# Kernel tuning notes

Measured on AMD Instinct MI355X. Metric: run time of the kernel, lower is better.

## Reference

```python
import jax, jax.numpy as jnp
import numpy as np

B, L, D, H, K_DELAYS = 8, 2048, 512, 8, 8
DH = D // H


def setup_inputs() -> dict:
    key = jax.random.key(0)
    ks = jax.random.split(key, 6)
    def lin_w(k):
        return 0.02 * jax.random.normal(k, (D, D), jnp.float32)
    return {
        "x_q":  jax.random.normal(ks[0], (B, L, D), jnp.float32),
        "x_kv": jax.random.normal(ks[1], (B, L, D), jnp.float32),
        "Wq": lin_w(ks[2]), "bq": jnp.zeros((D,), jnp.float32),
        "Wk": lin_w(ks[3]), "bk": jnp.zeros((D,), jnp.float32),
        "Wv": lin_w(ks[4]), "bv": jnp.zeros((D,), jnp.float32),
        "Wo": lin_w(ks[5]), "bo": jnp.zeros((D,), jnp.float32),
    }


def reference(x_q, x_kv, Wq, bq, Wk, bk, Wv, bv, Wo, bo):
    Bx, Lx, Dx = x_q.shape

    def proj(x, W, b):  # torch Linear: x @ W.T + b, then split heads -> [B,H,L,dh]
        return (x @ W.T + b).reshape(Bx, Lx, H, DH).transpose(0, 2, 1, 3)

    q = proj(x_q, Wq, bq)
    k = proj(x_kv, Wk, bk)
    v = proj(x_kv, Wv, bv)

    # FFT-based autocorrelation over the time axis (axis=2)
    qz = q - q.mean(axis=2, keepdims=True)
    kz = k - k.mean(axis=2, keepdims=True)
    Qf = jnp.fft.rfft(qz, axis=2)
    Kf = jnp.fft.rfft(kz, axis=2)
    corr = jnp.fft.irfft(Qf * jnp.conj(Kf), n=Lx, axis=2).mean(axis=-1)  # [B,H,L]
    # torch expands corr to [B,H,Lq,Lk] then means over Lq -> identical to corr
    score = corr

    K = min(K_DELAYS, Lx)
    vals, idx = jax.lax.top_k(score, K)                    # [B,H,K]
    w = vals / (vals.sum(axis=-1, keepdims=True) + 1e-12)
    w = jax.lax.stop_gradient(w)                           # .detach() in torch

    # circular shift by -delay == gather at (t + delay) mod L
    t = jnp.arange(Lx)
    pos = (t[None, None, None, :] + idx[..., None]) % Lx   # [B,H,K,L]
    v_sh = jnp.take_along_axis(v[:, :, None, :, :], pos[..., None], axis=3)  # [B,H,K,L,dh]
    out = jnp.einsum('bhk,bhkld->bhld', w, v_sh)           # weighted sum over delays

    out = out.transpose(0, 2, 1, 3).reshape(Bx, Lx, Dx)
    return out @ Wo.T + bo
```

## Files before the change

### kernel.cpp

```cpp
#include <hip/hip_runtime.h>
#include <math.h>

#define BB 8
#define LL 2048
#define DD 512
#define HH 8
#define DHH 64
#define KD 8
#define MM (BB*LL)

typedef _Float16 f16x2 __attribute__((ext_vector_type(2)));
typedef _Float16 f16x4 __attribute__((ext_vector_type(4)));
typedef _Float16 f16x8 __attribute__((ext_vector_type(8)));
typedef float    f32x4 __attribute__((ext_vector_type(4)));

__device__ inline void cvt8(const float* __restrict__ s, _Float16* hp, _Float16* lp) {
    const float4 a = *(const float4*)s;
    const float4 b = *(const float4*)(s + 4);
    const float v[8] = {a.x, a.y, a.z, a.w, b.x, b.y, b.z, b.w};
    f16x8 hi, lo;
#pragma unroll
    for (int j = 0; j < 8; j++) {
        const _Float16 h = (_Float16)v[j];
        hi[j] = h;
        lo[j] = (_Float16)((v[j] - (float)h) * 512.0f);
    }
    *(f16x8*)hp = hi;
    if (lp) *(f16x8*)lp = lo;
}

__global__ __launch_bounds__(256) void prep_w(const float* __restrict__ Wq, const float* __restrict__ Wk,
                                              const float* __restrict__ Wv, const float* __restrict__ Wo,
                                              _Float16* __restrict__ Wq_h, _Float16* __restrict__ Wq_l,
                                              _Float16* __restrict__ Wk_h, _Float16* __restrict__ Wk_l,
                                              _Float16* __restrict__ Wv_h, _Float16* __restrict__ Wo_h) {
    const int g = blockIdx.x * 256 + threadIdx.x;
    const int which = g >> 15;
    const size_t idx = (size_t)(g & 32767) * 8;
    if (which == 0)      cvt8(Wq + idx, Wq_h + idx, Wq_l + idx);
    else if (which == 1) cvt8(Wk + idx, Wk_h + idx, Wk_l + idx);
    else if (which == 2) cvt8(Wv + idx, Wv_h + idx, nullptr);
    else                 cvt8(Wo + idx, Wo_h + idx, nullptr);
}

__device__ __forceinline__ void stage16(const _Float16* g, const _Float16* l) {
    __builtin_amdgcn_global_load_lds(
        (const __attribute__((address_space(1))) void*)g,
        (__attribute__((address_space(3))) void*)l,
        16, 0, 0);
}

template<int NPROD, int MODE, int AF32, int BK>
__device__ __forceinline__ void gemm_body(const float* __restrict__ A32,
                                          const _Float16* __restrict__ Ag,
                                          const _Float16* __restrict__ Al_g,
                                          const _Float16* __restrict__ Bg,
                                          const _Float16* __restrict__ Bl_g,
                                          const float* __restrict__ bias,
                                          void* __restrict__ Cv,
                                          _Float16* lds, int l0) {
    constexpr int CPR  = BK / 8;
    constexpr int NST  = BK / 16;
    constexpr int SH   = (BK == 32) ? 2 : 3;
    constexpr int PLN  = 128 * BK;

#define SWZR(R) ((BK == 32) ? (((R) >> 1) & 3) : ((R) & 7))
#define ASWZ(R, g) ((size_t)(R) * BK + (size_t)((((g) ^ SWZR(R))) * 8))

    _Float16* Ah = lds;
    _Float16* Bh = lds + PLN;
    _Float16* Al = (NPROD == 3) ? lds + 2 * PLN : lds;
    _Float16* Bl = (NPROD == 3) ? lds + 3 * PLN : lds;

    const int t  = threadIdx.x;
    const int m0 = (((l0 >> 5) << 3) | (l0 & 7)) * 128;
    const int n0 = ((l0 >> 3) & 3) * 128;

    const int wv   = t >> 6;
    const int lane = t & 63;
    const int wm   = (wv >> 1) * 64;
    const int wn   = (wv & 1) * 64;
    const int lm   = lane & 15;
    const int quad = lane >> 4;

    int srow[NST], schk[NST], sgrp[NST];
#pragma unroll
    for (int i = 0; i < NST; i++) {
        const int s = (i * 4 + wv) * 64 + lane;
        srow[i] = s >> SH;
        schk[i] = (s & (CPR - 1)) ^ SWZR(srow[i]);
        sgrp[i] = (i * 4 + wv) * 512;
    }

    f32x4 acc0[4][4] = {};
    f32x4 acc1[4][4] = {};

    float4 vaA[NST], vaB[NST];
    if (AF32) {
#pragma unroll
        for (int i = 0; i < NST; i++) {
            const float* src = A32 + (size_t)(m0 + srow[i]) * 512 + schk[i] * 8;
            vaA[i] = *(const float4*)src;
            vaB[i] = *(const float4*)(src + 4);
        }
    }

    for (int k0 = 0; k0 < 512; k0 += BK) {
        __syncthreads();
#pragma unroll
        for (int i = 0; i < NST; i++) {
            const size_t offB = (size_t)(n0 + srow[i]) * 512 + k0 + schk[i] * 8;
            stage16(Bg + offB, Bh + sgrp[i]);
            if (NPROD == 3) stage16(Bl_g + offB, Bl + sgrp[i]);
            if (AF32) {
                const float va[8] = {vaA[i].x, vaA[i].y, vaA[i].z, vaA[i].w,
                                     vaB[i].x, vaB[i].y, vaB[i].z, vaB[i].w};
                f16x8 hi, lo;
#pragma unroll
                for (int j = 0; j < 8; j++) {
                    const _Float16 h = (_Float16)va[j];
                    hi[j] = h;
                    if (NPROD == 3) lo[j] = (_Float16)((va[j] - (float)h) * 512.0f);
                }
                *(f16x8*)&Ah[sgrp[i] + lane * 8] = hi;
                if (NPROD == 3) *(f16x8*)&Al[sgrp[i] + lane * 8] = lo;
            } else {
                const size_t offA = (size_t)(m0 + srow[i]) * 512 + k0 + schk[i] * 8;
                stage16(Ag + offA, Ah + sgrp[i]);
                if (NPROD == 3) stage16(Al_g + offA, Al + sgrp[i]);
            }
        }
        __syncthreads();

        if (AF32 && k0 + BK < 512) {
#pragma unroll
            for (int i = 0; i < NST; i++) {
                const float* src = A32 + (size_t)(m0 + srow[i]) * 512 + (k0 + BK) + schk[i] * 8;
                vaA[i] = *(const float4*)src;
                vaB[i] = *(const float4*)(src + 4);
            }
        }

#pragma unroll
        for (int ks = 0; ks < BK / 32; ks++) {
            const int gq = ks * 4 + quad;
            f16x8 afh[4], bf[4];
#pragma unroll
            for (int mt = 0; mt < 4; mt++)
                afh[mt] = *(f16x8*)&Ah[ASWZ(wm + mt * 16 + lm, gq)];
#pragma unroll
            for (int nt = 0; nt < 4; nt++)
                bf[nt] = *(f16x8*)&Bh[ASWZ(wn + nt * 16 + lm, gq)];

#pragma unroll
            for (int mt = 0; mt < 4; mt++)
#pragma unroll
                for (int nt = 0; nt < 4; nt++)
                    acc0[mt][nt] = __builtin_amdgcn_mfma_f32_16x16x32_f16(afh[mt], bf[nt], acc0[mt][nt], 0, 0, 0);

            if (NPROD == 3) {
                f16x8 afl[4];
#pragma unroll
                for (int mt = 0; mt < 4; mt++)
                    afl[mt] = *(f16x8*)&Al[ASWZ(wm + mt * 16 + lm, gq)];
#pragma unroll
                for (int mt = 0; mt < 4; mt++)
#pragma unroll
                    for (int nt = 0; nt < 4; nt++)
                        acc1[mt][nt] = __builtin_amdgcn_mfma_f32_16x16x32_f16(afl[mt], bf[nt], acc1[mt][nt], 0, 0, 0);
#pragma unroll
                for (int nt = 0; nt < 4; nt++)
                    bf[nt] = *(f16x8*)&Bl[ASWZ(wn + nt * 16 + lm, gq)];
#pragma unroll
                for (int mt = 0; mt < 4; mt++)
#pragma unroll
                    for (int nt = 0; nt < 4; nt++)
                        acc1[mt][nt] = __builtin_amdgcn_mfma_f32_16x16x32_f16(afh[mt], bf[nt], acc1[mt][nt], 0, 0, 0);
            }
        }
    }
#undef ASWZ
#undef SWZR

#pragma unroll
    for (int mt = 0; mt < 4; mt++) {
#pragma unroll
        for (int nt = 0; nt < 4; nt++) {
            const int n = n0 + wn + nt * 16 + lm;
            const float bv = bias[n];
            float val[4];
#pragma unroll
            for (int r = 0; r < 4; r++) {
                val[r] = acc0[mt][nt][r] + bv;
                if (NPROD == 3) val[r] += acc1[mt][nt][r] * (1.0f / 512.0f);
            }
            const int mbase = m0 + wm + mt * 16 + quad * 4;
            const int b_idx = mbase >> 11;
            const int lbase = mbase & 2047;
            if (MODE == 0) {
                float* C = (float*)Cv;
#pragma unroll
                for (int r = 0; r < 4; r++) C[(size_t)(mbase + r) * 512 + n] = val[r];
            } else if (MODE == 1) {
                float* C = (float*)Cv;
                float4 pv = make_float4(val[0], val[1], val[2], val[3]);
                *(float4*)&C[((size_t)(b_idx * 512 + n)) * 2048 + lbase] = pv;
            } else {
                _Float16* C = (_Float16*)Cv;
#pragma unroll
                for (int r = 0; r < 4; r++)
                    C[(size_t)b_idx * 1048576 + (size_t)(n >> 6) * 131072
                      + (size_t)(lbase + r) * 64 + (n & 63)] = (_Float16)val[r];
            }
        }
    }
}

__global__ __launch_bounds__(256, 2) void gemm_qk(const float* __restrict__ A0f,
                                                  const _Float16* __restrict__ B0h, const _Float16* __restrict__ B0l,
                                                  const float* __restrict__ bias0, float* __restrict__ C0,
                                                  const float* __restrict__ A1f,
                                                  const _Float16* __restrict__ B1h, const _Float16* __restrict__ B1l,
                                                  const float* __restrict__ bias1, float* __restrict__ C1) {
    __shared__ __align__(16) _Float16 lds[32768];
    const int prob = blockIdx.x >> 9;
    const int l0   = blockIdx.x & 511;
    if (prob == 0)
        gemm_body<3, 1, 1, 64>(A0f, nullptr, nullptr, B0h, B0l, bias0, C0, lds, l0);
    else
        gemm_body<3, 1, 1, 64>(A1f, nullptr, nullptr, B1h, B1l, bias1, C1, lds, l0);
}

__global__ __launch_bounds__(256, 3) void gemm_o(const _Float16* __restrict__ Ah_g,
                                                 const _Float16* __restrict__ Bh_g,
                                                 const float* __restrict__ bias,
                                                 float* __restrict__ C) {
    __shared__ __align__(16) _Float16 lds[16384];
    gemm_body<1, 0, 0, 64>(nullptr, Ah_g, Ah_g, Bh_g, Bh_g, bias, C, lds, blockIdx.x);
}

#define PAD3(i) ((i) + ((i) >> 3))

__device__ inline float2 cmul2(float2 a, float2 w) {
    return make_float2(a.x * w.x - a.y * w.y, a.x * w.y + a.y * w.x);
}
__device__ inline float2 cadd2(float2 a, float2 b) { return make_float2(a.x + b.x, a.y + b.y); }
__device__ inline float2 csub2(float2 a, float2 b) { return make_float2(a.x - b.x, a.y - b.y); }

__global__ __launch_bounds__(256) void fft_fwd(const float* __restrict__ qT,
                                               const float* __restrict__ kT,
                                               float* __restrict__ specP) {
    const int blk  = blockIdx.x;
    const int bh   = blk >> 4;
    const int part = blk & 15;
    const int t    = threadIdx.x;
    __shared__ float2 Zs[2304];
    __shared__ float2 Wt[1024];

#pragma unroll
    for (int s = 0; s < 4; s++) {
        const int j = t + s * 256;
        float sv, cv;
        __sincosf(2.0f * (float)M_PI * (float)j / 2048.0f, &sv, &cv);
        Wt[j] = make_float2(cv, -sv);
    }

    float2 pacc[8];
#pragma unroll
    for (int s = 0; s < 8; s++) pacc[s] = make_float2(0.0f, 0.0f);

    const int low5 = t & 31, hi3 = t >> 5;
    const int low2 = t & 3,  hi6 = t >> 2;

    float2 zn[8];
    {
        const int seq0 = bh * 64 + part * 4;
        const float* qp = qT + (size_t)seq0 * 2048;
        const float* kp = kT + (size_t)seq0 * 2048;
#pragma unroll
        for (int s = 0; s < 8; s++) zn[s] = make_float2(qp[t + 256 * s], kp[t + 256 * s]);
    }

    for (int j4 = 0; j4 < 4; j4++) {
        float2 z[8];
#pragma unroll
        for (int s = 0; s < 8; s++) z[s] = zn[s];
        if (j4 + 1 < 4) {
            const int seq = bh * 64 + part * 4 + j4 + 1;
            const float* qp = qT + (size_t)seq * 2048;
            const float* kp = kT + (size_t)seq * 2048;
#pragma unroll
            for (int s = 0; s < 8; s++) zn[s] = make_float2(qp[t + 256 * s], kp[t + 256 * s]);
        }
        __syncthreads();

#pragma unroll
        for (int sp = 0; sp < 4; sp++) {
            float2 u = z[sp], v = z[sp + 4];
            z[sp]     = cadd2(u, v);
            z[sp + 4] = cmul2(csub2(u, v), Wt[t + 256 * sp]);
        }
#pragma unroll
        for (int base = 0; base < 8; base += 4)
#pragma unroll
            for (int q2 = 0; q2 < 2; q2++) {
                float2 u = z[base + q2], v = z[base + q2 + 2];
                z[base + q2]     = cadd2(u, v);
                z[base + q2 + 2] = cmul2(csub2(u, v), Wt[2 * (t + 256 * q2)]);
            }
        {
            const float2 w = Wt[4 * t];
#pragma unroll
            for (int e = 0; e < 8; e += 2) {
                float2 u = z[e], v = z[e + 1];
                z[e]     = cadd2(u, v);
                z[e + 1] = cmul2(csub2(u, v), w);
            }
        }

#pragma unroll
        for (int s = 0; s < 8; s++) Zs[PAD3(t + 256 * s)] = z[s];
        __syncthreads();
#pragma unroll
        for (int s = 0; s < 8; s++) z[s] = Zs[PAD3(low5 + 32 * s + 256 * hi3)];

#pragma unroll
        for (int sp = 0; sp < 4; sp++) {
            float2 u = z[sp], v = z[sp + 4];
            z[sp]     = cadd2(u, v);
            z[sp + 4] = cmul2(csub2(u, v), Wt[8 * (low5 + 32 * sp)]);
        }
#pragma unroll
        for (int base = 0; base < 8; base += 4)
#pragma unroll
            for (int q2 = 0; q2 < 2; q2++) {
                float2 u = z[base + q2], v = z[base + q2 + 2];
                z[base + q2]     = cadd2(u, v);
                z[base + q2 + 2] = cmul2(csub2(u, v), Wt[16 * (low5 + 32 * q2)]);
            }
        {
            const float2 w = Wt[32 * low5];
#pragma unroll
            for (int e = 0; e < 8; e += 2) {
                float2 u = z[e], v = z[e + 1];
                z[e]     = cadd2(u, v);
                z[e + 1] = cmul2(csub2(u, v), w);
            }
        }

#pragma unroll
        for (int s = 0; s < 8; s++) Zs[PAD3(low5 + 32 * s + 256 * hi3)] = z[s];
        __syncthreads();
#pragma unroll
        for (int s = 0; s < 8; s++) z[s] = Zs[PAD3(low2 + 4 * s + 32 * hi6)];

#pragma unroll
        for (int sp = 0; sp < 4; sp++) {
            float2 u = z[sp], v = z[sp + 4];
            z[sp]     = cadd2(u, v);
            z[sp + 4] = cmul2(csub2(u, v), Wt[64 * (low2 + 4 * sp)]);
        }
#pragma unroll
        for (int base = 0; base < 8; base += 4)
#pragma unroll
            for (int q2 = 0; q2 < 2; q2++) {
                float2 u = z[base + q2], v = z[base + q2 + 2];
                z[base + q2]     = cadd2(u, v);
                z[base + q2 + 2] = cmul2(csub2(u, v), Wt[128 * (low2 + 4 * q2)]);
            }
        {
            const float2 w = Wt[256 * low2];
#pragma unroll
            for (int e = 0; e < 8; e += 2) {
                float2 u = z[e], v = z[e + 1];
                z[e]     = cadd2(u, v);
                z[e + 1] = cmul2(csub2(u, v), w);
            }
        }

#pragma unroll
        for (int s = 0; s < 8; s++) Zs[PAD3(low2 + 4 * s + 32 * hi6)] = z[s];
        __syncthreads();
#pragma unroll
        for (int s = 0; s < 8; s++) z[s] = Zs[PAD3(8 * t + s)];

#pragma unroll
        for (int base = 0; base < 8; base += 4) {
            {
                float2 u = z[base], v = z[base + 2];
                z[base]     = cadd2(u, v);
                z[base + 2] = csub2(u, v);
            }
            {
                float2 u = z[base + 1], v = z[base + 3];
                float2 d = csub2(u, v);
                z[base + 1] = cadd2(u, v);
                z[base + 3] = make_float2(d.y, -d.x);
            }
        }
#pragma unroll
        for (int e = 0; e < 8; e += 2) {
            float2 u = z[e], v = z[e + 1];
            z[e]     = cadd2(u, v);
            z[e + 1] = csub2(u, v);
        }

#pragma unroll
        for (int s = 0; s < 8; s++) Zs[PAD3(8 * t + s)] = z[s];
        __syncthreads();

#pragma unroll
        for (int s = 0; s < 8; s++) {
            const int p  = t + 256 * s;
            const int f  = (int)(__brev((unsigned)p) >> 21);
            const int fm = (2048 - f) & 2047;
            const int p2 = (int)(__brev((unsigned)fm) >> 21);
            const float2 zf = Zs[PAD3(p)];
            const float2 zm = Zs[PAD3(p2)];
            const float qr = 0.5f * (zf.x + zm.x);
            const float qi = 0.5f * (zf.y - zm.y);
            const float kr = 0.5f * (zf.y + zm.y);
            const float ki = 0.5f * (zm.x - zf.x);
            if (f != 0) {
                pacc[s].x += qr * kr + qi * ki;
                pacc[s].y += qi * kr - qr * ki;
            }
        }
    }

    float2* outp = (float2*)specP + (size_t)blk * 2048;
#pragma unroll
    for (int s = 0; s < 8; s++) outp[t + 256 * s] = pacc[s];
}

__device__ inline void build_twiddle(float2* Wt, int tid, float sign) {
#pragma unroll
    for (int s = 0; s < 4; s++) {
        const int j = tid + s * 256;
        const float a = 2.0f * (float)M_PI * (float)j / 2048.0f;
        float sv, cv;
        __sincosf(a, &sv, &cv);
        Wt[j] = make_float2(cv, sign * sv);
    }
}

__device__ inline void fft2048_stages(float2* Z, const float2* Wt, int tid) {
    for (int st = 0; st < 11; st++) {
        const int half = 1 << st;
        const int shift = 10 - st;
#pragma unroll
        for (int r = 0; r < 4; r++) {
            const int m   = tid + r * 256;
            const int grp = m >> st;
            const int pos = m & (half - 1);
            const int i0  = (grp << (st + 1)) + pos;
            const int i1  = i0 + half;
            const float2 w = Wt[pos << shift];
            const float2 a = Z[i0];
            const float2 b = Z[i1];
            const float tr = b.x * w.x - b.y * w.y;
            const float ti = b.x * w.y + b.y * w.x;
            Z[i0] = make_float2(a.x + tr, a.y + ti);
            Z[i1] = make_float2(a.x - tr, a.y - ti);
        }
        __syncthreads();
    }
}

__global__ __launch_bounds__(256, 3) void gemm_v_fftinv(const float* __restrict__ xkv,
                                                        const _Float16* __restrict__ Bh_g,
                                                        const float* __restrict__ bias,
                                                        _Float16* __restrict__ C,
                                                        const float* __restrict__ specP,
                                                        int* __restrict__ delays,
                                                        float* __restrict__ weights) {
    __shared__ __align__(16) char smem[24608];
    const int bid = blockIdx.x;
    const int tid = threadIdx.x;

    if (bid >= 64) {
        gemm_body<1, 2, 1, 32>(xkv, nullptr, nullptr, Bh_g, Bh_g, bias, C, (_Float16*)smem, bid - 64);
        return;
    }

    const int bh = bid;
    float2* Z  = (float2*)smem;
    float2* Wt = (float2*)(smem + 16384);
    float*  wvs = (float*)(smem + 24576);
    int*    wis = (int*)(smem + 24592);

    build_twiddle(Wt, tid, +1.0f);

    const float2* sp = (const float2*)specP + (size_t)bh * 16 * 2048;
#pragma unroll
    for (int s = 0; s < 8; s++) {
        const int p = tid + s * 256;
        float2 acc = make_float2(0.0f, 0.0f);
#pragma unroll
        for (int part = 0; part < 16; part++) {
            const float2 v = sp[part * 2048 + p];
            acc.x += v.x; acc.y += v.y;
        }
        Z[p] = acc;
    }
    __syncthreads();
    fft2048_stages(Z, Wt, tid);

    const float scale = 1.0f / (2048.0f * 64.0f);
    float cv[8];
#pragma unroll
    for (int s = 0; s < 8; s++) cv[s] = Z[tid + s * 256].x * scale;

    float bkv[KD];
    int   bki[KD];
#pragma unroll
    for (int k = 0; k < KD; k++) {
        float lv = -1e30f;
        int   li = 1 << 30;
#pragma unroll
        for (int s = 0; s < 8; s++) {
            const int idx = tid + s * 256;
            if (cv[s] > lv || (cv[s] == lv && idx < li)) { lv = cv[s]; li = idx; }
        }
#pragma unroll
        for (int off = 1; off < 64; off <<= 1) {
            const float v2 = __shfl_xor(lv, off);
            const int   i2 = __shfl_xor(li, off);
            if (v2 > lv || (v2 == lv && i2 < li)) { lv = v2; li = i2; }
        }
        if ((tid & 63) == 0) { wvs[tid >> 6] = lv; wis[tid >> 6] = li; }
        __syncthreads();
        float bv = wvs[0];
        int   bi = wis[0];
#pragma unroll
        for (int j = 1; j < 4; j++) {
            const float v2 = wvs[j];
            const int   i2 = wis[j];
            if (v2 > bv || (v2 == bv && i2 < bi)) { bv = v2; bi = i2; }
        }
        bkv[k] = bv;
        bki[k] = bi;
        if ((bi & 255) == tid) {
            const int slot = bi >> 8;
#pragma unroll
            for (int s = 0; s < 8; s++)
                if (s == slot) cv[s] = -1e30f;
        }
        __syncthreads();
    }

    if (tid == 0) {
        float sum = 0.0f;
#pragma unroll
        for (int k = 0; k < KD; k++) sum += bkv[k];
        const float inv = 1.0f / (sum + 1e-12f);
#pragma unroll
        for (int k = 0; k < KD; k++) {
            weights[bh * KD + k] = bkv[k] * inv;
            delays[bh * KD + k]  = bki[k];
        }
    }
}

__global__ __launch_bounds__(256) void gather_ws(const _Float16* __restrict__ v,
                                                 const int* __restrict__ delays,
                                                 const float* __restrict__ weights,
                                                 _Float16* __restrict__ outb) {
    const int gp = blockIdx.x * 256 + threadIdx.x;
    const int c8 = gp & 63;
    const int m  = gp >> 6;
    const int l  = m & 2047;
    const int b  = m >> 11;
    const int ch = c8 * 8;
    const int h  = ch >> 6;
    const int dh = ch & 63;
    const int bh = b * 8 + h;

    const _Float16* vb = v + (size_t)bh * 131072;
    float a[8] = {};
#pragma unroll
    for (int k = 0; k < KD; k++) {
        const int   d = delays[bh * KD + k];
        const float w = weights[bh * KD + k];
        const int   p = (l + d) & 2047;
        const f16x8 pv = *(const f16x8*)&vb[p * 64 + dh];
#pragma unroll
        for (int j = 0; j < 8; j++) a[j] = fmaf(w, (float)pv[j], a[j]);
    }
    f16x8 ov;
#pragma unroll
    for (int j = 0; j < 8; j++) ov[j] = (_Float16)a[j];
    *(f16x8*)&outb[(size_t)m * 512 + ch] = ov;
}

extern "C" void kernel_launch(void* const* d_in, const int* in_sizes, int n_in,
                              void* d_out, int out_size, void* d_ws, size_t ws_size,
                              hipStream_t stream) {
    const float* x_q  = (const float*)d_in[0];
    const float* x_kv = (const float*)d_in[1];
    const float* Wq   = (const float*)d_in[2];
    const float* bq   = (const float*)d_in[3];
    const float* Wk   = (const float*)d_in[4];
    const float* bk   = (const float*)d_in[5];
    const float* Wv   = (const float*)d_in[6];
    const float* bv   = (const float*)d_in[7];
    const float* Wo   = (const float*)d_in[8];
    const float* bo   = (const float*)d_in[9];
    float* out = (float*)d_out;

    char* ws = (char*)d_ws;
    float*    kf32  = (float*)   (ws + 0);
    _Float16* vh    = (_Float16*)(ws + 33554432);
    float*    specP = (float*)   (ws + 50331648);
    _Float16* gbuf  = (_Float16*)(ws + 67108864);
    _Float16* Wq_h  = (_Float16*)(ws + 83886080);
    _Float16* Wq_l  = (_Float16*)(ws + 84410368);
    _Float16* Wk_h  = (_Float16*)(ws + 84934656);
    _Float16* Wk_l  = (_Float16*)(ws + 85458944);
    _Float16* Wv_h  = (_Float16*)(ws + 85983232);
    _Float16* Wo_h  = (_Float16*)(ws + 86507520);
    int*      dely  = (int*)     (ws + 87031808);
    float*    wgt   = (float*)   (ws + 87033856);
    float*    qf32  = (float*)d_out;

    dim3 blk(256);

    prep_w<<<dim3(512), blk, 0, stream>>>(Wq, Wk, Wv, Wo,
                                          Wq_h, Wq_l, Wk_h, Wk_l, Wv_h, Wo_h);

    gemm_qk<<<dim3(1024), blk, 0, stream>>>(x_q,  Wq_h, Wq_l, bq, qf32,
                                            x_kv, Wk_h, Wk_l, bk, kf32);

    fft_fwd<<<dim3(1024), blk, 0, stream>>>(qf32, kf32, specP);

    gemm_v_fftinv<<<dim3(576), blk, 0, stream>>>(x_kv, Wv_h, bv, vh, specP, dely, wgt);

    gather_ws<<<dim3(4096), blk, 0, stream>>>(vh, dely, wgt, gbuf);

    gemm_o<<<dim3(512), blk, 0, stream>>>(gbuf, Wo_h, bo, out);
}
```

Baseline: 255.0 us.

## Fuse weight conversion into QK projection GEMM and drop prep kernel

The separate prep_w kernel is removed. The Q/K projection GEMM now reads fp32 weights directly and splits them into hi/lo fp16 in registers before writing to LDS, the same way it already handles the activations. Wv/Wo conversion runs in 256 extra blocks appended to the gemm_qk grid. This saves one kernel launch and the round trip of the converted Q/K weights through memory, but every GEMM block now redoes the weight conversion and issues twice as many fp32 B loads.

```diff
diff --git a/kernel.cpp b/kernel.cpp
--- a/kernel.cpp
+++ b/kernel.cpp
@@ -29,20 +29,6 @@
     if (lp) *(f16x8*)lp = lo;
 }
 
-__global__ __launch_bounds__(256) void prep_w(const float* __restrict__ Wq, const float* __restrict__ Wk,
-                                              const float* __restrict__ Wv, const float* __restrict__ Wo,
-                                              _Float16* __restrict__ Wq_h, _Float16* __restrict__ Wq_l,
-                                              _Float16* __restrict__ Wk_h, _Float16* __restrict__ Wk_l,
-                                              _Float16* __restrict__ Wv_h, _Float16* __restrict__ Wo_h) {
-    const int g = blockIdx.x * 256 + threadIdx.x;
-    const int which = g >> 15;
-    const size_t idx = (size_t)(g & 32767) * 8;
-    if (which == 0)      cvt8(Wq + idx, Wq_h + idx, Wq_l + idx);
-    else if (which == 1) cvt8(Wk + idx, Wk_h + idx, Wk_l + idx);
-    else if (which == 2) cvt8(Wv + idx, Wv_h + idx, nullptr);
-    else                 cvt8(Wo + idx, Wo_h + idx, nullptr);
-}
-
 __device__ __forceinline__ void stage16(const _Float16* g, const _Float16* l) {
     __builtin_amdgcn_global_load_lds(
         (const __attribute__((address_space(1))) void*)g,
@@ -50,10 +36,11 @@
         16, 0, 0);
 }
 
-template<int NPROD, int MODE, int AF32, int BK>
+template<int NPROD, int MODE, int AF32, int BF32, int BK>
 __device__ __forceinline__ void gemm_body(const float* __restrict__ A32,
                                           const _Float16* __restrict__ Ag,
                                           const _Float16* __restrict__ Al_g,
+                                          const float* __restrict__ B32,
                                           const _Float16* __restrict__ Bg,
                                           const _Float16* __restrict__ Bl_g,
                                           const float* __restrict__ bias,
@@ -95,7 +82,7 @@
     f32x4 acc0[4][4] = {};
     f32x4 acc1[4][4] = {};
 
-    float4 vaA[NST], vaB[NST];
+    float4 vaA[NST], vaB[NST], vbA[NST], vbB[NST];
     if (AF32) {
 #pragma unroll
         for (int i = 0; i < NST; i++) {
@@ -104,14 +91,36 @@
             vaB[i] = *(const float4*)(src + 4);
         }
     }
+    if (BF32) {
+#pragma unroll
+        for (int i = 0; i < NST; i++) {
+            const float* src = B32 + (size_t)(n0 + srow[i]) * 512 + schk[i] * 8;
+            vbA[i] = *(const float4*)src;
+            vbB[i] = *(const float4*)(src + 4);
+        }
+    }
 
     for (int k0 = 0; k0 < 512; k0 += BK) {
         __syncthreads();
 #pragma unroll
         for (int i = 0; i < NST; i++) {
-            const size_t offB = (size_t)(n0 + srow[i]) * 512 + k0 + schk[i] * 8;
-            stage16(Bg + offB, Bh + sgrp[i]);
-            if (NPROD == 3) stage16(Bl_g + offB, Bl + sgrp[i]);
+            if (BF32) {
+                const float vb[8] = {vbA[i].x, vbA[i].y, vbA[i].z, vbA[i].w,
+                                     vbB[i].x, vbB[i].y, vbB[i].z, vbB[i].w};
+                f16x8 hi, lo;
+#pragma unroll
+                for (int j = 0; j < 8; j++) {
+                    const _Float16 h = (_Float16)vb[j];
+                    hi[j] = h;
+                    if (NPROD == 3) lo[j] = (_Float16)((vb[j] - (float)h) * 512.0f);
+                }
+                *(f16x8*)&Bh[sgrp[i] + lane * 8] = hi;
+                if (NPROD == 3) *(f16x8*)&Bl[sgrp[i] + lane * 8] = lo;
+            } else {
+                const size_t offB = (size_t)(n0 + srow[i]) * 512 + k0 + schk[i] * 8;
+                stage16(Bg + offB, Bh + sgrp[i]);
+                if (NPROD == 3) stage16(Bl_g + offB, Bl + sgrp[i]);
+            }
             if (AF32) {
                 const float va[8] = {vaA[i].x, vaA[i].y, vaA[i].z, vaA[i].w,
                                      vaB[i].x, vaB[i].y, vaB[i].z, vaB[i].w};
@@ -132,12 +141,22 @@
         }
         __syncthreads();
 
-        if (AF32 && k0 + BK < 512) {
-#pragma unroll
-            for (int i = 0; i < NST; i++) {
-                const float* src = A32 + (size_t)(m0 + srow[i]) * 512 + (k0 + BK) + schk[i] * 8;
-                vaA[i] = *(const float4*)src;
-                vaB[i] = *(const float4*)(src + 4);
+        if (k0 + BK < 512) {
+            if (AF32) {
+#pragma unroll
+                for (int i = 0; i < NST; i++) {
+                    const float* src = A32 + (size_t)(m0 + srow[i]) * 512 + (k0 + BK) + schk[i] * 8;
+                    vaA[i] = *(const float4*)src;
+                    vaB[i] = *(const float4*)(src + 4);
+                }
+            }
+            if (BF32) {
+#pragma unroll
+                for (int i = 0; i < NST; i++) {
+                    const float* src = B32 + (size_t)(n0 + srow[i]) * 512 + (k0 + BK) + schk[i] * 8;
+                    vbA[i] = *(const float4*)src;
+                    vbB[i] = *(const float4*)(src + 4);
+                }
             }
         }
 
@@ -217,18 +236,29 @@
 }
 
 __global__ __launch_bounds__(256, 2) void gemm_qk(const float* __restrict__ A0f,
-                                                  const _Float16* __restrict__ B0h, const _Float16* __restrict__ B0l,
+                                                  const float* __restrict__ W0f,
                                                   const float* __restrict__ bias0, float* __restrict__ C0,
                                                   const float* __restrict__ A1f,
-                                                  const _Float16* __restrict__ B1h, const _Float16* __restrict__ B1l,
-                                                  const float* __restrict__ bias1, float* __restrict__ C1) {
+                                                  const float* __restrict__ W1f,
+                                                  const float* __restrict__ bias1, float* __restrict__ C1,
+                                                  const float* __restrict__ Wv, const float* __restrict__ Wo,
+                                                  _Float16* __restrict__ Wv_h, _Float16* __restrict__ Wo_h) {
     __shared__ __align__(16) _Float16 lds[32768];
-    const int prob = blockIdx.x >> 9;
-    const int l0   = blockIdx.x & 511;
+    const int bid = blockIdx.x;
+    if (bid >= 1024) {
+        const int g = (bid - 1024) * 256 + threadIdx.x;
+        const int which = g >> 15;
+        const size_t idx = (size_t)(g & 32767) * 8;
+        if (which == 0) cvt8(Wv + idx, Wv_h + idx, nullptr);
+        else            cvt8(Wo + idx, Wo_h + idx, nullptr);
+        return;
+    }
+    const int prob = bid >> 9;
+    const int l0   = bid & 511;
     if (prob == 0)
-        gemm_body<3, 1, 1, 64>(A0f, nullptr, nullptr, B0h, B0l, bias0, C0, lds, l0);
+        gemm_body<3, 1, 1, 1, 64>(A0f, nullptr, nullptr, W0f, nullptr, nullptr, bias0, C0, lds, l0);
     else
-        gemm_body<3, 1, 1, 64>(A1f, nullptr, nullptr, B1h, B1l, bias1, C1, lds, l0);
+        gemm_body<3, 1, 1, 1, 64>(A1f, nullptr, nullptr, W1f, nullptr, nullptr, bias1, C1, lds, l0);
 }
 
 __global__ __launch_bounds__(256, 3) void gemm_o(const _Float16* __restrict__ Ah_g,
@@ -236,7 +266,7 @@
                                                  const float* __restrict__ bias,
                                                  float* __restrict__ C) {
     __shared__ __align__(16) _Float16 lds[16384];
-    gemm_body<1, 0, 0, 64>(nullptr, Ah_g, Ah_g, Bh_g, Bh_g, bias, C, lds, blockIdx.x);
+    gemm_body<1, 0, 0, 0, 64>(nullptr, Ah_g, Ah_g, nullptr, Bh_g, Bh_g, bias, C, lds, blockIdx.x);
 }
 
 #define PAD3(i) ((i) + ((i) >> 3))
@@ -479,7 +509,8 @@
     const int tid = threadIdx.x;
 
     if (bid >= 64) {
-        gemm_body<1, 2, 1, 32>(xkv, nullptr, nullptr, Bh_g, Bh_g, bias, C, (_Float16*)smem, bid - 64);
+        gemm_body<1, 2, 1, 0, 32>(xkv, nullptr, nullptr, nullptr, Bh_g, Bh_g, bias, C,
+                                  (_Float16*)smem, bid - 64);
         return;
     }
 
@@ -613,23 +644,17 @@
     _Float16* vh    = (_Float16*)(ws + 33554432);
     float*    specP = (float*)   (ws + 50331648);
     _Float16* gbuf  = (_Float16*)(ws + 67108864);
-    _Float16* Wq_h  = (_Float16*)(ws + 83886080);
-    _Float16* Wq_l  = (_Float16*)(ws + 84410368);
-    _Float16* Wk_h  = (_Float16*)(ws + 84934656);
-    _Float16* Wk_l  = (_Float16*)(ws + 85458944);
-    _Float16* Wv_h  = (_Float16*)(ws + 85983232);
-    _Float16* Wo_h  = (_Float16*)(ws + 86507520);
-    int*      dely  = (int*)     (ws + 87031808);
-    float*    wgt   = (float*)   (ws + 87033856);
+    _Float16* Wv_h  = (_Float16*)(ws + 83886080);
+    _Float16* Wo_h  = (_Float16*)(ws + 84410368);
+    int*      dely  = (int*)     (ws + 84934656);
+    float*    wgt   = (float*)   (ws + 84936704);
     float*    qf32  = (float*)d_out;
 
     dim3 blk(256);
 
-    prep_w<<<dim3(512), blk, 0, stream>>>(Wq, Wk, Wv, Wo,
-                                          Wq_h, Wq_l, Wk_h, Wk_l, Wv_h, Wo_h);
-
-    gemm_qk<<<dim3(1024), blk, 0, stream>>>(x_q,  Wq_h, Wq_l, bq, qf32,
-                                            x_kv, Wk_h, Wk_l, bk, kf32);
+    gemm_qk<<<dim3(1280), blk, 0, stream>>>(x_q,  Wq, bq, qf32,
+                                            x_kv, Wk, bk, kf32,
+                                            Wv, Wo, Wv_h, Wo_h);
 
     fft_fwd<<<dim3(1024), blk, 0, stream>>>(qf32, kf32, specP);
 
```

Result: slower. 270.5 us (+6.1%).
